# Kernel optimization log

Measured on AMD Instinct MI355X. Metric: run time of the kernel, lower is better.

Reference implementation:

```python
import jax, jax.numpy as jnp
import numpy as np

NUM_NODES = 10000
NUM_EDGES = 640000
D_FEAT = 128

def setup_inputs() -> dict:
    key = jax.random.key(0)
    k1, k2 = jax.random.split(key)
    x = jax.random.normal(k1, (NUM_NODES, D_FEAT), dtype=jnp.float32)
    edge_index = jax.random.randint(k2, (2, NUM_EDGES), 0, NUM_NODES, dtype=jnp.int64)
    return {"x": x, "edge_index": edge_index}

def reference(x, edge_index):
    # MessagePassing(aggr='add') with default message/update:
    # msg = x[src]; out[n] = sum of msg over edges with dst == n
    src, dst = edge_index[0], edge_index[1]
    msg = x[src]                                   # [num_edges, d]
    out = jax.ops.segment_sum(msg, dst, num_segments=NUM_NODES)  # [num_nodes, d]
    return out
```

## Files before the change

### kernel.cpp

```cpp
#include <hip/hip_runtime.h>

#define NUM_NODES 10000
#define NUM_EDGES 640000
#define D_FEAT 128

#define NPB 20
#define NB 500
#define K1_BLOCKS 256
#define EPB (NUM_EDGES / K1_BLOCKS)
#define CELL_CAP 16
#define MAXB 1664

#define XB_U4 (NUM_NODES * 16)
#define CVT_PER_BLOCK (XB_U4 / K1_BLOCKS)


__device__ __forceinline__ unsigned bf16_rne(float f) {
    unsigned u = __float_as_uint(f);
    return (u + 0x7FFFu + ((u >> 16) & 1u)) >> 16;
}

__device__ __forceinline__ int bucket_of(int d) {
    return (int)(((unsigned)d * 104858u) >> 21);
}

__global__ __launch_bounds__(1024) void scatter_cvt_kernel(
    const int* __restrict__ ei, const float4* __restrict__ x4,
    uint4* __restrict__ xb, unsigned* __restrict__ cnt,
    unsigned* __restrict__ ovfcell, uint4* __restrict__ slots4)
{
    __shared__ int cur[NB];
    __shared__ uint4 cellsv[NB * (CELL_CAP / 4)];
    __shared__ unsigned s_ovf[16];
    __shared__ int ovfcur;

    int t = threadIdx.x, b = blockIdx.x;
    if (t < NB) cur[t] = 0;
    if (t < 16) s_ovf[t] = 0xFFFFFFFFu;
    if (t == 0) ovfcur = 0;

    int base = b * EPB;
    int s0 = ei[base + t];
    int d0 = ei[NUM_EDGES + base + t];
    int s1 = ei[base + t + 1024];
    int d1 = ei[NUM_EDGES + base + t + 1024];
    int s2 = 0, d2 = 0;
    bool has2 = (t + 2048) < EPB;
    if (has2) {
        s2 = ei[base + t + 2048];
        d2 = ei[NUM_EDGES + base + t + 2048];
    }

    if (t < CVT_PER_BLOCK) {
        int o = b * CVT_PER_BLOCK + t;
        float4 a = x4[2 * o];
        float4 c = x4[2 * o + 1];
        uint4 w;
        w.x = bf16_rne(a.x) | (bf16_rne(a.y) << 16);
        w.y = bf16_rne(a.z) | (bf16_rne(a.w) << 16);
        w.z = bf16_rne(c.x) | (bf16_rne(c.y) << 16);
        w.w = bf16_rne(c.z) | (bf16_rne(c.w) << 16);
        xb[o] = w;
    }
    __syncthreads();

    unsigned* cells = (unsigned*)cellsv;
    {
        int k = bucket_of(d0), m = d0 - k * NPB;
        int pos = atomicAdd(&cur[k], 1);
        if (pos < CELL_CAP)
            cells[k * CELL_CAP + pos] = ((unsigned)m << 16) | (unsigned)s0;
        else {
            int o = atomicAdd(&ovfcur, 1);
            if (o < 16) s_ovf[o] = ((unsigned)k << 19) |
                                   ((unsigned)m << 14) | (unsigned)s0;
        }
    }
    {
        int k = bucket_of(d1), m = d1 - k * NPB;
        int pos = atomicAdd(&cur[k], 1);
        if (pos < CELL_CAP)
            cells[k * CELL_CAP + pos] = ((unsigned)m << 16) | (unsigned)s1;
        else {
            int o = atomicAdd(&ovfcur, 1);
            if (o < 16) s_ovf[o] = ((unsigned)k << 19) |
                                   ((unsigned)m << 14) | (unsigned)s1;
        }
    }
    if (has2) {
        int k = bucket_of(d2), m = d2 - k * NPB;
        int pos = atomicAdd(&cur[k], 1);
        if (pos < CELL_CAP)
            cells[k * CELL_CAP + pos] = ((unsigned)m << 16) | (unsigned)s2;
        else {
            int o = atomicAdd(&ovfcur, 1);
            if (o < 16) s_ovf[o] = ((unsigned)k << 19) |
                                   ((unsigned)m << 14) | (unsigned)s2;
        }
    }
    __syncthreads();

    for (int idx = t; idx < NB * (CELL_CAP / 4); idx += 1024) {
        int k = idx >> 2, j = idx & 3;
        slots4[((unsigned)k * K1_BLOCKS + (unsigned)b) * (CELL_CAP / 4) + j] =
            cellsv[idx];
    }
    if (t < NB) cnt[b * NB + t] = (unsigned)cur[t];
    if (t < 16) ovfcell[b * 16 + t] = s_ovf[t];
}

__device__ __forceinline__ void acc8(float* a, uint4 w) {
    a[0] += __uint_as_float(w.x << 16);
    a[1] += __uint_as_float(w.x & 0xFFFF0000u);
    a[2] += __uint_as_float(w.y << 16);
    a[3] += __uint_as_float(w.y & 0xFFFF0000u);
    a[4] += __uint_as_float(w.z << 16);
    a[5] += __uint_as_float(w.z & 0xFFFF0000u);
    a[6] += __uint_as_float(w.w << 16);
    a[7] += __uint_as_float(w.w & 0xFFFF0000u);
}

__global__ __launch_bounds__(640, 5) void sort_gather_kernel(
    const uint4* __restrict__ xb,
    const unsigned* __restrict__ cnt,
    const uint4* __restrict__ slots4,
    const unsigned* __restrict__ ovfcell,
    float4* __restrict__ out4)
{
    __shared__ int s_cnt[K1_BLOCKS];
    __shared__ unsigned s_src[MAXB];
    __shared__ int h[NPB];
    __shared__ int off20[NPB];
    __shared__ int cur20[NPB];

    int k = blockIdx.x;
    int t = threadIdx.x;

    if (t < NPB) h[t] = 0;
    if (t < K1_BLOCKS) s_cnt[t] = (int)cnt[t * NB + k];
    __syncthreads();

    const uint4* sb = slots4 + (unsigned)k * (K1_BLOCKS * CELL_CAP / 4);
    uint4 w40, w41 = make_uint4(0u, 0u, 0u, 0u);
    int vc0, vc1 = 0;
    {
        int c = t >> 2, su = t & 3;
        w40 = sb[t];
        int v = min(s_cnt[c], CELL_CAP) - su * 4;
        vc0 = max(0, min(4, v));
    }
    if (t < 384) {
        int idx = t + 640;
        int c = idx >> 2, su = idx & 3;
        w41 = sb[idx];
        int v = min(s_cnt[c], CELL_CAP) - su * 4;
        vc1 = max(0, min(4, v));
    }
    if (vc0 > 0) atomicAdd(&h[w40.x >> 16], 1);
    if (vc0 > 1) atomicAdd(&h[w40.y >> 16], 1);
    if (vc0 > 2) atomicAdd(&h[w40.z >> 16], 1);
    if (vc0 > 3) atomicAdd(&h[w40.w >> 16], 1);
    if (vc1 > 0) atomicAdd(&h[w41.x >> 16], 1);
    if (vc1 > 1) atomicAdd(&h[w41.y >> 16], 1);
    if (vc1 > 2) atomicAdd(&h[w41.z >> 16], 1);
    if (vc1 > 3) atomicAdd(&h[w41.w >> 16], 1);
    if (t < K1_BLOCKS && s_cnt[t] > CELL_CAP) {
        for (int i = 0; i < 16; ++i) {
            unsigned e = ovfcell[t * 16 + i];
            if ((int)(e >> 19) == k) atomicAdd(&h[(e >> 14) & 31u], 1);
        }
    }
    __syncthreads();

    if (t < 32) {
        int val = (t < NPB) ? h[t] : 0;
        int s = val;
        #pragma unroll
        for (int d = 1; d < 32; d <<= 1) {
            int u = __shfl_up(s, d, 32);
            if (t >= d) s += u;
        }
        if (t < NPB) { off20[t] = s - val; cur20[t] = s - val; }
    }
    __syncthreads();

    if (vc0 > 0) { int p = atomicAdd(&cur20[w40.x >> 16], 1); if (p < MAXB) s_src[p] = w40.x & 0xFFFFu; }
    if (vc0 > 1) { int p = atomicAdd(&cur20[w40.y >> 16], 1); if (p < MAXB) s_src[p] = w40.y & 0xFFFFu; }
    if (vc0 > 2) { int p = atomicAdd(&cur20[w40.z >> 16], 1); if (p < MAXB) s_src[p] = w40.z & 0xFFFFu; }
    if (vc0 > 3) { int p = atomicAdd(&cur20[w40.w >> 16], 1); if (p < MAXB) s_src[p] = w40.w & 0xFFFFu; }
    if (vc1 > 0) { int p = atomicAdd(&cur20[w41.x >> 16], 1); if (p < MAXB) s_src[p] = w41.x & 0xFFFFu; }
    if (vc1 > 1) { int p = atomicAdd(&cur20[w41.y >> 16], 1); if (p < MAXB) s_src[p] = w41.y & 0xFFFFu; }
    if (vc1 > 2) { int p = atomicAdd(&cur20[w41.z >> 16], 1); if (p < MAXB) s_src[p] = w41.z & 0xFFFFu; }
    if (vc1 > 3) { int p = atomicAdd(&cur20[w41.w >> 16], 1); if (p < MAXB) s_src[p] = w41.w & 0xFFFFu; }
    if (t < K1_BLOCKS && s_cnt[t] > CELL_CAP) {
        for (int i = 0; i < 16; ++i) {
            unsigned e = ovfcell[t * 16 + i];
            if ((int)(e >> 19) == k) {
                int p = atomicAdd(&cur20[(e >> 14) & 31u], 1);
                if (p < MAXB) s_src[p] = e & 0x3FFFu;
            }
        }
    }
    __syncthreads();

    int wave = t >> 6;
    int lane = t & 63;
    int q    = lane >> 4;
    int sub  = lane & 15;

    #pragma unroll
    for (int mm = 0; mm < 2; ++mm) {
        int m = wave * 2 + mm;
        int beg = off20[m], ec = h[m];
        int last = ec > 0 ? ec - 1 : 0;

        float a[8] = {0.f, 0.f, 0.f, 0.f, 0.f, 0.f, 0.f, 0.f};

        bool val = q < ec;
        unsigned i0 = (unsigned)min(beg + min(q, last), MAXB - 1);
        uint4 wv = xb[(s_src[i0] & 0xFFFFu) * 16u + (unsigned)sub];

        for (int j = 0; j < ec; j += 4) {
            int jn = j + 4;
            unsigned i1 = (unsigned)min(beg + min(jn + q, last), MAXB - 1);
            uint4 wv1 = xb[(s_src[i1] & 0xFFFFu) * 16u + (unsigned)sub];
            bool val1 = (jn + q) < ec;
            if (val) acc8(a, wv);
            wv = wv1; val = val1;
        }

        #pragma unroll
        for (int r = 0; r < 8; ++r) {
            a[r] += __shfl_down(a[r], 32);
            a[r] += __shfl_down(a[r], 16);
        }
        if (q == 0) {
            unsigned o = (unsigned)(k * NPB + m) * 32u + (unsigned)sub * 2u;
            out4[o]     = make_float4(a[0], a[1], a[2], a[3]);
            out4[o + 1] = make_float4(a[4], a[5], a[6], a[7]);
        }
    }
}

extern "C" void kernel_launch(void* const* d_in, const int* in_sizes, int n_in,
                              void* d_out, int out_size, void* d_ws, size_t ws_size,
                              hipStream_t stream) {
    const float* x   = (const float*)d_in[0];
    const int*   ei  = (const int*)d_in[1];
    float*       out = (float*)d_out;

    uint4*    xb      = (uint4*)d_ws;
    unsigned* cnt     = (unsigned*)(xb + XB_U4);
    unsigned* ovfcell = cnt + K1_BLOCKS * NB;
    uint4*    slots4  = (uint4*)(ovfcell + K1_BLOCKS * 16);

    scatter_cvt_kernel<<<K1_BLOCKS, 1024, 0, stream>>>(
        ei, (const float4*)x, xb, cnt, ovfcell, slots4);

    sort_gather_kernel<<<NB, 640, 0, stream>>>(
        xb, cnt, (const uint4*)slots4, ovfcell, (float4*)out);
}
```

Measured before the change: 81.24 us.

## Split fused sort+gather into separate sort and per-node gather kernels

The combined bucket-sort and gather kernel becomes two kernels. The sort kernel writes each bucket's sorted source list and per-node offset/count to global memory. A new gather kernel then runs one wave per node over 2500 small blocks, with source-index prefetch two steps ahead. This is meant to improve load balance and occupancy in the gather phase, at the cost of an extra launch and a global round trip for the sorted indices.

Result: slower. 85.39 us (+5.1%).

```diff
diff --git a/kernel.cpp b/kernel.cpp
--- a/kernel.cpp
+++ b/kernel.cpp
@@ -10,6 +10,7 @@
 #define EPB (NUM_EDGES / K1_BLOCKS)
 #define CELL_CAP 16
 #define MAXB 1664
+#define NIW 32
 
 #define XB_U4 (NUM_NODES * 16)
 #define CVT_PER_BLOCK (XB_U4 / K1_BLOCKS)
@@ -20,7 +21,7 @@
     return (u + 0x7FFFu + ((u >> 16) & 1u)) >> 16;
 }
 
-__device__ __forceinline__ int bucket_of(int d) {
+__device__ __forceinline__ int div20(int d) {
     return (int)(((unsigned)d * 104858u) >> 21);
 }
 
@@ -66,7 +67,7 @@
 
     unsigned* cells = (unsigned*)cellsv;
     {
-        int k = bucket_of(d0), m = d0 - k * NPB;
+        int k = div20(d0), m = d0 - k * NPB;
         int pos = atomicAdd(&cur[k], 1);
         if (pos < CELL_CAP)
             cells[k * CELL_CAP + pos] = ((unsigned)m << 16) | (unsigned)s0;
@@ -77,7 +78,7 @@
         }
     }
     {
-        int k = bucket_of(d1), m = d1 - k * NPB;
+        int k = div20(d1), m = d1 - k * NPB;
         int pos = atomicAdd(&cur[k], 1);
         if (pos < CELL_CAP)
             cells[k * CELL_CAP + pos] = ((unsigned)m << 16) | (unsigned)s1;
@@ -88,7 +89,7 @@
         }
     }
     if (has2) {
-        int k = bucket_of(d2), m = d2 - k * NPB;
+        int k = div20(d2), m = d2 - k * NPB;
         int pos = atomicAdd(&cur[k], 1);
         if (pos < CELL_CAP)
             cells[k * CELL_CAP + pos] = ((unsigned)m << 16) | (unsigned)s2;
@@ -109,23 +110,12 @@
     if (t < 16) ovfcell[b * 16 + t] = s_ovf[t];
 }
 
-__device__ __forceinline__ void acc8(float* a, uint4 w) {
-    a[0] += __uint_as_float(w.x << 16);
-    a[1] += __uint_as_float(w.x & 0xFFFF0000u);
-    a[2] += __uint_as_float(w.y << 16);
-    a[3] += __uint_as_float(w.y & 0xFFFF0000u);
-    a[4] += __uint_as_float(w.z << 16);
-    a[5] += __uint_as_float(w.z & 0xFFFF0000u);
-    a[6] += __uint_as_float(w.w << 16);
-    a[7] += __uint_as_float(w.w & 0xFFFF0000u);
-}
-
-__global__ __launch_bounds__(640, 5) void sort_gather_kernel(
-    const uint4* __restrict__ xb,
+__global__ __launch_bounds__(640, 5) void sort_kernel(
     const unsigned* __restrict__ cnt,
     const uint4* __restrict__ slots4,
     const unsigned* __restrict__ ovfcell,
-    float4* __restrict__ out4)
+    unsigned* __restrict__ seg,
+    unsigned* __restrict__ nodeinfo)
 {
     __shared__ int s_cnt[K1_BLOCKS];
     __shared__ unsigned s_src[MAXB];
@@ -203,42 +193,72 @@
     }
     __syncthreads();
 
-    int wave = t >> 6;
-    int lane = t & 63;
-    int q    = lane >> 4;
-    int sub  = lane & 15;
+    int ntot = min(off20[NPB - 1] + h[NPB - 1], MAXB);
+    for (int i = t; i < ntot; i += 640)
+        seg[(unsigned)k * MAXB + (unsigned)i] = s_src[i];
+    if (t < NPB)
+        nodeinfo[k * NIW + t] =
+            ((unsigned)off20[t] << 16) | (unsigned)min(h[t], 0xFFFF);
+}
+
+__device__ __forceinline__ void acc8(float* a, uint4 w) {
+    a[0] += __uint_as_float(w.x << 16);
+    a[1] += __uint_as_float(w.x & 0xFFFF0000u);
+    a[2] += __uint_as_float(w.y << 16);
+    a[3] += __uint_as_float(w.y & 0xFFFF0000u);
+    a[4] += __uint_as_float(w.z << 16);
+    a[5] += __uint_as_float(w.z & 0xFFFF0000u);
+    a[6] += __uint_as_float(w.w << 16);
+    a[7] += __uint_as_float(w.w & 0xFFFF0000u);
+}
+
+__global__ __launch_bounds__(256) void gather_kernel(
+    const uint4* __restrict__ xb,
+    const unsigned* __restrict__ seg,
+    const unsigned* __restrict__ nodeinfo,
+    float4* __restrict__ out4)
+{
+    int wave = threadIdx.x >> 6;
+    int lane = threadIdx.x & 63;
+    int n = blockIdx.x * 4 + wave;
+    int k = div20(n), m = n - k * NPB;
+
+    unsigned info = nodeinfo[k * NIW + m];
+    int beg = (int)(info >> 16);
+    int ec  = (int)(info & 0xFFFFu);
+    int last = ec > 0 ? ec - 1 : 0;
+
+    const unsigned* sl = seg + (unsigned)k * MAXB;
+    int q   = lane >> 4;
+    int sub = lane & 15;
+
+    float a[8] = {0.f, 0.f, 0.f, 0.f, 0.f, 0.f, 0.f, 0.f};
+
+    unsigned i0 = (unsigned)min(beg + min(0 + q, last), MAXB - 1);
+    unsigned i4 = (unsigned)min(beg + min(4 + q, last), MAXB - 1);
+    unsigned sA = sl[i0];
+    unsigned sB = sl[i4];
+    uint4 r = xb[(sA & 0xFFFFu) * 16u + (unsigned)sub];
+    bool v = q < ec;
+
+    for (int j = 0; j < ec; j += 4) {
+        unsigned ic = (unsigned)min(beg + min(j + 8 + q, last), MAXB - 1);
+        unsigned sC = sl[ic];
+        uint4 r1 = xb[(sB & 0xFFFFu) * 16u + (unsigned)sub];
+        bool v1 = (j + 4 + q) < ec;
+        if (v) acc8(a, r);
+        r = r1; v = v1; sB = sC;
+    }
 
     #pragma unroll
-    for (int mm = 0; mm < 2; ++mm) {
-        int m = wave * 2 + mm;
-        int beg = off20[m], ec = h[m];
-        int last = ec > 0 ? ec - 1 : 0;
-
-        float a[8] = {0.f, 0.f, 0.f, 0.f, 0.f, 0.f, 0.f, 0.f};
-
-        bool val = q < ec;
-        unsigned i0 = (unsigned)min(beg + min(q, last), MAXB - 1);
-        uint4 wv = xb[(s_src[i0] & 0xFFFFu) * 16u + (unsigned)sub];
-
-        for (int j = 0; j < ec; j += 4) {
-            int jn = j + 4;
-            unsigned i1 = (unsigned)min(beg + min(jn + q, last), MAXB - 1);
-            uint4 wv1 = xb[(s_src[i1] & 0xFFFFu) * 16u + (unsigned)sub];
-            bool val1 = (jn + q) < ec;
-            if (val) acc8(a, wv);
-            wv = wv1; val = val1;
-        }
-
-        #pragma unroll
-        for (int r = 0; r < 8; ++r) {
-            a[r] += __shfl_down(a[r], 32);
-            a[r] += __shfl_down(a[r], 16);
-        }
-        if (q == 0) {
-            unsigned o = (unsigned)(k * NPB + m) * 32u + (unsigned)sub * 2u;
-            out4[o]     = make_float4(a[0], a[1], a[2], a[3]);
-            out4[o + 1] = make_float4(a[4], a[5], a[6], a[7]);
-        }
+    for (int rr = 0; rr < 8; ++rr) {
+        a[rr] += __shfl_down(a[rr], 32);
+        a[rr] += __shfl_down(a[rr], 16);
+    }
+    if (q == 0) {
+        unsigned o = (unsigned)n * 32u + (unsigned)sub * 2u;
+        out4[o]     = make_float4(a[0], a[1], a[2], a[3]);
+        out4[o + 1] = make_float4(a[4], a[5], a[6], a[7]);
     }
 }
 
@@ -249,14 +269,20 @@
     const int*   ei  = (const int*)d_in[1];
     float*       out = (float*)d_out;
 
-    uint4*    xb      = (uint4*)d_ws;
-    unsigned* cnt     = (unsigned*)(xb + XB_U4);
-    unsigned* ovfcell = cnt + K1_BLOCKS * NB;
-    uint4*    slots4  = (uint4*)(ovfcell + K1_BLOCKS * 16);
+    uint4*    xb       = (uint4*)d_ws;
+    unsigned* cnt      = (unsigned*)(xb + XB_U4);
+    unsigned* ovfcell  = cnt + K1_BLOCKS * NB;
+    uint4*    slots4   = (uint4*)(ovfcell + K1_BLOCKS * 16);
+    unsigned* seg      = (unsigned*)(slots4 +
+                         (size_t)NB * K1_BLOCKS * (CELL_CAP / 4));
+    unsigned* nodeinfo = seg + (size_t)NB * MAXB;
 
     scatter_cvt_kernel<<<K1_BLOCKS, 1024, 0, stream>>>(
         ei, (const float4*)x, xb, cnt, ovfcell, slots4);
 
-    sort_gather_kernel<<<NB, 640, 0, stream>>>(
-        xb, cnt, (const uint4*)slots4, ovfcell, (float4*)out);
-}
+    sort_kernel<<<NB, 640, 0, stream>>>(
+        cnt, (const uint4*)slots4, ovfcell, seg, nodeinfo);
+
+    gather_kernel<<<NUM_NODES / 4, 256, 0, stream>>>(
+        xb, seg, nodeinfo, (float4*)out);
+}
```

## Replace per-cell count array with sentinel-marked slots and padded zero-row gather

Applied to the files above, without the earlier changes.

The scatter kernel now pre-fills its shared cells with an invalid sentinel, so the separate per-block count array no longer has to be written or read. The sort kernel finds valid entries by checking the sentinel, and it scans overflow entries only when some block reported overflow. Each node's source list is padded to a multiple of four with an index to an extra all-zero row, so the gather loop drops its per-iteration clamps and validity checks. In exchange it adds some wasted gathers of the zero row, extra shared-memory initialisation, and reorders which waves handle which nodes.

Result: no change. 81.59 us (+0.4%).

```diff
diff --git a/kernel.cpp b/kernel.cpp
--- a/kernel.cpp
+++ b/kernel.cpp
@@ -9,10 +9,12 @@
 #define K1_BLOCKS 256
 #define EPB (NUM_EDGES / K1_BLOCKS)
 #define CELL_CAP 16
-#define MAXB 1664
-
-#define XB_U4 (NUM_NODES * 16)
-#define CVT_PER_BLOCK (XB_U4 / K1_BLOCKS)
+#define MAXB 1792
+#define INV 0xFFFFFFFFu
+#define ZROW 10000u
+
+#define XB_U4 (NUM_NODES * 16 + 16)
+#define CVT_PER_BLOCK (NUM_NODES * 16 / K1_BLOCKS)
 
 
 __device__ __forceinline__ unsigned bf16_rne(float f) {
@@ -20,24 +22,26 @@
     return (u + 0x7FFFu + ((u >> 16) & 1u)) >> 16;
 }
 
-__device__ __forceinline__ int bucket_of(int d) {
+__device__ __forceinline__ int div20(int d) {
     return (int)(((unsigned)d * 104858u) >> 21);
 }
 
 __global__ __launch_bounds__(1024) void scatter_cvt_kernel(
     const int* __restrict__ ei, const float4* __restrict__ x4,
-    uint4* __restrict__ xb, unsigned* __restrict__ cnt,
-    unsigned* __restrict__ ovfcell, uint4* __restrict__ slots4)
+    uint4* __restrict__ xb, unsigned* __restrict__ ovfcell,
+    uint4* __restrict__ slots4)
 {
     __shared__ int cur[NB];
     __shared__ uint4 cellsv[NB * (CELL_CAP / 4)];
-    __shared__ unsigned s_ovf[16];
+    __shared__ unsigned s_ovf[15];
     __shared__ int ovfcur;
 
     int t = threadIdx.x, b = blockIdx.x;
     if (t < NB) cur[t] = 0;
-    if (t < 16) s_ovf[t] = 0xFFFFFFFFu;
+    if (t < 15) s_ovf[t] = 0;
     if (t == 0) ovfcur = 0;
+    uint4 iv = make_uint4(INV, INV, INV, INV);
+    if (t < 1000) { cellsv[t] = iv; cellsv[t + 1000] = iv; }
 
     int base = b * EPB;
     int s0 = ei[base + t];
@@ -62,51 +66,51 @@
         w.w = bf16_rne(c.z) | (bf16_rne(c.w) << 16);
         xb[o] = w;
     }
+    if (b == 0 && t < 16)
+        xb[NUM_NODES * 16 + t] = make_uint4(0u, 0u, 0u, 0u);
     __syncthreads();
 
     unsigned* cells = (unsigned*)cellsv;
     {
-        int k = bucket_of(d0), m = d0 - k * NPB;
+        int k = div20(d0), m = d0 - k * NPB;
         int pos = atomicAdd(&cur[k], 1);
         if (pos < CELL_CAP)
             cells[k * CELL_CAP + pos] = ((unsigned)m << 16) | (unsigned)s0;
         else {
             int o = atomicAdd(&ovfcur, 1);
-            if (o < 16) s_ovf[o] = ((unsigned)k << 19) |
+            if (o < 15) s_ovf[o] = ((unsigned)k << 19) |
                                    ((unsigned)m << 14) | (unsigned)s0;
         }
     }
     {
-        int k = bucket_of(d1), m = d1 - k * NPB;
+        int k = div20(d1), m = d1 - k * NPB;
         int pos = atomicAdd(&cur[k], 1);
         if (pos < CELL_CAP)
             cells[k * CELL_CAP + pos] = ((unsigned)m << 16) | (unsigned)s1;
         else {
             int o = atomicAdd(&ovfcur, 1);
-            if (o < 16) s_ovf[o] = ((unsigned)k << 19) |
+            if (o < 15) s_ovf[o] = ((unsigned)k << 19) |
                                    ((unsigned)m << 14) | (unsigned)s1;
         }
     }
     if (has2) {
-        int k = bucket_of(d2), m = d2 - k * NPB;
+        int k = div20(d2), m = d2 - k * NPB;
         int pos = atomicAdd(&cur[k], 1);
         if (pos < CELL_CAP)
             cells[k * CELL_CAP + pos] = ((unsigned)m << 16) | (unsigned)s2;
         else {
             int o = atomicAdd(&ovfcur, 1);
-            if (o < 16) s_ovf[o] = ((unsigned)k << 19) |
+            if (o < 15) s_ovf[o] = ((unsigned)k << 19) |
                                    ((unsigned)m << 14) | (unsigned)s2;
         }
     }
     __syncthreads();
 
-    for (int idx = t; idx < NB * (CELL_CAP / 4); idx += 1024) {
-        int k = idx >> 2, j = idx & 3;
-        slots4[((unsigned)k * K1_BLOCKS + (unsigned)b) * (CELL_CAP / 4) + j] =
-            cellsv[idx];
-    }
-    if (t < NB) cnt[b * NB + t] = (unsigned)cur[t];
-    if (t < 16) ovfcell[b * 16 + t] = s_ovf[t];
+    for (int idx = t; idx < NB * (CELL_CAP / 4); idx += 1024)
+        slots4[((unsigned)(idx >> 2) * K1_BLOCKS + (unsigned)b) *
+               (CELL_CAP / 4) + (unsigned)(idx & 3)] = cellsv[idx];
+    if (t < 15) ovfcell[b * 16 + t] = s_ovf[t];
+    if (t == 15) ovfcell[b * 16 + 15] = (unsigned)min(ovfcur, 15);
 }
 
 __device__ __forceinline__ void acc8(float* a, uint4 w) {
@@ -120,52 +124,63 @@
     a[7] += __uint_as_float(w.w & 0xFFFF0000u);
 }
 
+__device__ __forceinline__ void reduce_write(float* a, int node, int q, int sub,
+                                             float4* __restrict__ out4) {
+    #pragma unroll
+    for (int r = 0; r < 8; ++r) {
+        a[r] += __shfl_down(a[r], 32);
+        a[r] += __shfl_down(a[r], 16);
+    }
+    if (q == 0) {
+        unsigned o = (unsigned)node * 32u + (unsigned)sub * 2u;
+        out4[o]     = make_float4(a[0], a[1], a[2], a[3]);
+        out4[o + 1] = make_float4(a[4], a[5], a[6], a[7]);
+    }
+}
+
 __global__ __launch_bounds__(640, 5) void sort_gather_kernel(
     const uint4* __restrict__ xb,
-    const unsigned* __restrict__ cnt,
     const uint4* __restrict__ slots4,
     const unsigned* __restrict__ ovfcell,
     float4* __restrict__ out4)
 {
-    __shared__ int s_cnt[K1_BLOCKS];
     __shared__ unsigned s_src[MAXB];
     __shared__ int h[NPB];
     __shared__ int off20[NPB];
     __shared__ int cur20[NPB];
+    __shared__ int s_ovfany;
 
     int k = blockIdx.x;
     int t = threadIdx.x;
 
     if (t < NPB) h[t] = 0;
-    if (t < K1_BLOCKS) s_cnt[t] = (int)cnt[t * NB + k];
-    __syncthreads();
-
-    const uint4* sb = slots4 + (unsigned)k * (K1_BLOCKS * CELL_CAP / 4);
-    uint4 w40, w41 = make_uint4(0u, 0u, 0u, 0u);
-    int vc0, vc1 = 0;
-    {
-        int c = t >> 2, su = t & 3;
-        w40 = sb[t];
-        int v = min(s_cnt[c], CELL_CAP) - su * 4;
-        vc0 = max(0, min(4, v));
-    }
-    if (t < 384) {
-        int idx = t + 640;
-        int c = idx >> 2, su = idx & 3;
-        w41 = sb[idx];
-        int v = min(s_cnt[c], CELL_CAP) - su * 4;
-        vc1 = max(0, min(4, v));
-    }
-    if (vc0 > 0) atomicAdd(&h[w40.x >> 16], 1);
-    if (vc0 > 1) atomicAdd(&h[w40.y >> 16], 1);
-    if (vc0 > 2) atomicAdd(&h[w40.z >> 16], 1);
-    if (vc0 > 3) atomicAdd(&h[w40.w >> 16], 1);
-    if (vc1 > 0) atomicAdd(&h[w41.x >> 16], 1);
-    if (vc1 > 1) atomicAdd(&h[w41.y >> 16], 1);
-    if (vc1 > 2) atomicAdd(&h[w41.z >> 16], 1);
-    if (vc1 > 3) atomicAdd(&h[w41.w >> 16], 1);
-    if (t < K1_BLOCKS && s_cnt[t] > CELL_CAP) {
-        for (int i = 0; i < 16; ++i) {
+    if (t == 0) s_ovfany = 0;
+    for (int i = t; i < MAXB; i += 640) s_src[i] = ZROW;
+
+    if (t < K1_BLOCKS) {
+        unsigned oc = ovfcell[t * 16 + 15];
+        if (oc) atomicOr(&s_ovfany, 1);
+    }
+
+    const uint4* sb = slots4 + (unsigned)k * 1024u;
+    uint4 w40 = sb[t];
+    uint4 w41 = (t < 384) ? sb[t + 640] : make_uint4(INV, INV, INV, INV);
+    __syncthreads();
+
+    {
+        unsigned m;
+        m = w40.x >> 16; if (m < NPB) atomicAdd(&h[m], 1);
+        m = w40.y >> 16; if (m < NPB) atomicAdd(&h[m], 1);
+        m = w40.z >> 16; if (m < NPB) atomicAdd(&h[m], 1);
+        m = w40.w >> 16; if (m < NPB) atomicAdd(&h[m], 1);
+        m = w41.x >> 16; if (m < NPB) atomicAdd(&h[m], 1);
+        m = w41.y >> 16; if (m < NPB) atomicAdd(&h[m], 1);
+        m = w41.z >> 16; if (m < NPB) atomicAdd(&h[m], 1);
+        m = w41.w >> 16; if (m < NPB) atomicAdd(&h[m], 1);
+    }
+    if (s_ovfany && t < K1_BLOCKS) {
+        int oc = (int)min(ovfcell[t * 16 + 15], 15u);
+        for (int i = 0; i < oc; ++i) {
             unsigned e = ovfcell[t * 16 + i];
             if ((int)(e >> 19) == k) atomicAdd(&h[(e >> 14) & 31u], 1);
         }
@@ -173,7 +188,7 @@
     __syncthreads();
 
     if (t < 32) {
-        int val = (t < NPB) ? h[t] : 0;
+        int val = (t < NPB) ? (((h[t] + 3) & ~3) + 4) : 0;
         int s = val;
         #pragma unroll
         for (int d = 1; d < 32; d <<= 1) {
@@ -184,16 +199,20 @@
     }
     __syncthreads();
 
-    if (vc0 > 0) { int p = atomicAdd(&cur20[w40.x >> 16], 1); if (p < MAXB) s_src[p] = w40.x & 0xFFFFu; }
-    if (vc0 > 1) { int p = atomicAdd(&cur20[w40.y >> 16], 1); if (p < MAXB) s_src[p] = w40.y & 0xFFFFu; }
-    if (vc0 > 2) { int p = atomicAdd(&cur20[w40.z >> 16], 1); if (p < MAXB) s_src[p] = w40.z & 0xFFFFu; }
-    if (vc0 > 3) { int p = atomicAdd(&cur20[w40.w >> 16], 1); if (p < MAXB) s_src[p] = w40.w & 0xFFFFu; }
-    if (vc1 > 0) { int p = atomicAdd(&cur20[w41.x >> 16], 1); if (p < MAXB) s_src[p] = w41.x & 0xFFFFu; }
-    if (vc1 > 1) { int p = atomicAdd(&cur20[w41.y >> 16], 1); if (p < MAXB) s_src[p] = w41.y & 0xFFFFu; }
-    if (vc1 > 2) { int p = atomicAdd(&cur20[w41.z >> 16], 1); if (p < MAXB) s_src[p] = w41.z & 0xFFFFu; }
-    if (vc1 > 3) { int p = atomicAdd(&cur20[w41.w >> 16], 1); if (p < MAXB) s_src[p] = w41.w & 0xFFFFu; }
-    if (t < K1_BLOCKS && s_cnt[t] > CELL_CAP) {
-        for (int i = 0; i < 16; ++i) {
+    {
+        unsigned m;
+        m = w40.x >> 16; if (m < NPB) { int p = atomicAdd(&cur20[m], 1); if (p < MAXB) s_src[p] = w40.x & 0xFFFFu; }
+        m = w40.y >> 16; if (m < NPB) { int p = atomicAdd(&cur20[m], 1); if (p < MAXB) s_src[p] = w40.y & 0xFFFFu; }
+        m = w40.z >> 16; if (m < NPB) { int p = atomicAdd(&cur20[m], 1); if (p < MAXB) s_src[p] = w40.z & 0xFFFFu; }
+        m = w40.w >> 16; if (m < NPB) { int p = atomicAdd(&cur20[m], 1); if (p < MAXB) s_src[p] = w40.w & 0xFFFFu; }
+        m = w41.x >> 16; if (m < NPB) { int p = atomicAdd(&cur20[m], 1); if (p < MAXB) s_src[p] = w41.x & 0xFFFFu; }
+        m = w41.y >> 16; if (m < NPB) { int p = atomicAdd(&cur20[m], 1); if (p < MAXB) s_src[p] = w41.y & 0xFFFFu; }
+        m = w41.z >> 16; if (m < NPB) { int p = atomicAdd(&cur20[m], 1); if (p < MAXB) s_src[p] = w41.z & 0xFFFFu; }
+        m = w41.w >> 16; if (m < NPB) { int p = atomicAdd(&cur20[m], 1); if (p < MAXB) s_src[p] = w41.w & 0xFFFFu; }
+    }
+    if (s_ovfany && t < K1_BLOCKS) {
+        int oc = (int)min(ovfcell[t * 16 + 15], 15u);
+        for (int i = 0; i < oc; ++i) {
             unsigned e = ovfcell[t * 16 + i];
             if ((int)(e >> 19) == k) {
                 int p = atomicAdd(&cur20[(e >> 14) & 31u], 1);
@@ -208,37 +227,35 @@
     int q    = lane >> 4;
     int sub  = lane & 15;
 
-    #pragma unroll
-    for (int mm = 0; mm < 2; ++mm) {
-        int m = wave * 2 + mm;
-        int beg = off20[m], ec = h[m];
-        int last = ec > 0 ? ec - 1 : 0;
-
+    {
+        int m = wave;
+        int bA = off20[m];
+        int eA = (h[m] + 3) & ~3;
         float a[8] = {0.f, 0.f, 0.f, 0.f, 0.f, 0.f, 0.f, 0.f};
-
-        bool val = q < ec;
-        unsigned i0 = (unsigned)min(beg + min(q, last), MAXB - 1);
-        uint4 wv = xb[(s_src[i0] & 0xFFFFu) * 16u + (unsigned)sub];
-
-        for (int j = 0; j < ec; j += 4) {
-            int jn = j + 4;
-            unsigned i1 = (unsigned)min(beg + min(jn + q, last), MAXB - 1);
-            uint4 wv1 = xb[(s_src[i1] & 0xFFFFu) * 16u + (unsigned)sub];
-            bool val1 = (jn + q) < ec;
-            if (val) acc8(a, wv);
-            wv = wv1; val = val1;
-        }
-
-        #pragma unroll
-        for (int r = 0; r < 8; ++r) {
-            a[r] += __shfl_down(a[r], 32);
-            a[r] += __shfl_down(a[r], 16);
-        }
-        if (q == 0) {
-            unsigned o = (unsigned)(k * NPB + m) * 32u + (unsigned)sub * 2u;
-            out4[o]     = make_float4(a[0], a[1], a[2], a[3]);
-            out4[o + 1] = make_float4(a[4], a[5], a[6], a[7]);
-        }
+        unsigned s = s_src[bA + q];
+        uint4 r = xb[s * 16u + (unsigned)sub];
+        for (int j = 0; j < eA; j += 4) {
+            unsigned s2 = s_src[bA + j + 4 + q];
+            uint4 r2 = xb[s2 * 16u + (unsigned)sub];
+            acc8(a, r);
+            r = r2;
+        }
+        reduce_write(a, k * NPB + m, q, sub, out4);
+    }
+    {
+        int m = wave + 10;
+        int bB = off20[m];
+        int eB = (h[m] + 3) & ~3;
+        float a[8] = {0.f, 0.f, 0.f, 0.f, 0.f, 0.f, 0.f, 0.f};
+        unsigned s = s_src[bB + q];
+        uint4 r = xb[s * 16u + (unsigned)sub];
+        for (int j = 0; j < eB; j += 4) {
+            unsigned s2 = s_src[bB + j + 4 + q];
+            uint4 r2 = xb[s2 * 16u + (unsigned)sub];
+            acc8(a, r);
+            r = r2;
+        }
+        reduce_write(a, k * NPB + m, q, sub, out4);
     }
 }
 
@@ -250,13 +267,12 @@
     float*       out = (float*)d_out;
 
     uint4*    xb      = (uint4*)d_ws;
-    unsigned* cnt     = (unsigned*)(xb + XB_U4);
-    unsigned* ovfcell = cnt + K1_BLOCKS * NB;
+    unsigned* ovfcell = (unsigned*)(xb + XB_U4);
     uint4*    slots4  = (uint4*)(ovfcell + K1_BLOCKS * 16);
 
     scatter_cvt_kernel<<<K1_BLOCKS, 1024, 0, stream>>>(
-        ei, (const float4*)x, xb, cnt, ovfcell, slots4);
+        ei, (const float4*)x, xb, ovfcell, slots4);
 
     sort_gather_kernel<<<NB, 640, 0, stream>>>(
-        xb, cnt, (const uint4*)slots4, ovfcell, (float4*)out);
-}
+        xb, (const uint4*)slots4, ovfcell, (float4*)out);
+}
```
